# Kernel optimization log

Hardware: AMD Instinct MI355X
Metric: run time of the kernel (lower is better)

The kernel has to match this reference:

```python
import jax, jax.numpy as jnp
import numpy as np

M, K, N = 131072, 1024, 512


def setup_inputs() -> dict:
    key = jax.random.key(0)
    k1, k2, k3, k4, k5 = jax.random.split(key, 5)
    scale = 0.02
    return {
        "x": jax.random.normal(k1, (M, K), dtype=jnp.float32),
        "w0": jax.random.uniform(k2, (K,), dtype=jnp.float32, minval=0.9, maxval=1.1),
        "w1": jax.random.normal(k3, (K, N), dtype=jnp.float32) * scale,
        "w2": jax.random.normal(k4, (K, N), dtype=jnp.float32) * scale,
        "w3": jax.random.normal(k5, (N, K), dtype=jnp.float32) * scale,
    }


def reference(x, w0, w1, w2, w3):
    # RMSNorm (no eps, matching the kernel): l = rsqrt(mean(x^2))
    l = jax.lax.rsqrt(jnp.sum(x * x, axis=-1) / K)          # [M]
    x1 = x * l[:, None] * w0[None, :]                        # [M, K]
    x2 = x1 @ w1                                             # gate   [M, N]
    y2 = x1 @ w2                                             # up     [M, N]
    x3 = jax.nn.silu(x2) * y2                                # SiLU-gate [M, N]
    out = x3 @ w3                                            # down   [M, K] (skip_connection=False)
    return out
```

## Files before the change

kernel.cpp:

```cpp
#include <hip/hip_runtime.h>
#include <cstdint>

typedef __attribute__((ext_vector_type(4))) float f32x4;
typedef __attribute__((ext_vector_type(8))) short bf16x8;
typedef __attribute__((ext_vector_type(4))) short bf16x4;

#define DEV static __device__ __forceinline__

DEV unsigned short f2bf(float f) {
    union { float f; unsigned int u; } v; v.f = f;
    unsigned int u = v.u;
    return (unsigned short)((u + 0x7FFFu + ((u >> 16) & 1u)) >> 16);
}

DEV void async_cp16(const void* g, void* l) {
    __builtin_amdgcn_global_load_lds(
        (const __attribute__((address_space(1))) unsigned int*)g,
        (__attribute__((address_space(3))) unsigned int*)l,
        16, 0, 0);
}

DEV void stage_half(const unsigned short* __restrict__ g, long kofs,
                    unsigned short* l, int tid, int gpitch) {
#pragma unroll
    for (int i = 0; i < 2; ++i) {
        int c = i * 512 + tid;
        int row = c >> 3;
        int ss = (c & 7) ^ (row & 7);
        async_cp16(g + (long)row * gpitch + kofs + ss * 8,
                   l + (i * 512 + (tid & 448)) * 8);
    }
}

DEV bf16x8 ldsrd(const unsigned short* base, int r, int q) {
    return *(const bf16x8*)&base[r * 64 + ((q ^ (r & 7)) << 3)];
}

template <int NT>
DEV void gemm256(const unsigned short* __restrict__ gA,
                 const unsigned short* __restrict__ gB,
                 const int gpitch, unsigned short* lds,
                 f32x4 (&acc)[8][4], const int tid) {
    const int lane = tid & 63;
    const int wv = tid >> 6;
    const int wr = wv >> 2;
    const int wcq = wv & 3;
    const int lhi = lane >> 4, llo = lane & 15;
    const int hb = wcq >> 1;
    const int br0 = (wcq & 1) * 64;

#define MG(AF, BF, KQ, RI0, CJ0)                                              \
    _Pragma("unroll") for (int i = 0; i < 4; ++i)                             \
    _Pragma("unroll") for (int j = 0; j < 2; ++j)                             \
        acc[RI0 + i][CJ0 + j] = __builtin_amdgcn_mfma_f32_16x16x32_bf16(      \
            AF[KQ][i], BF[KQ][j], acc[RI0 + i][CJ0 + j], 0, 0, 0);

    stage_half(gA, 0, lds + 0 * 8192, tid, gpitch);
    stage_half(gA + (long)128 * gpitch, 0, lds + 1 * 8192, tid, gpitch);
    stage_half(gB, 0, lds + 32768 + 0 * 8192, tid, gpitch);
    stage_half(gB + (long)128 * gpitch, 0, lds + 32768 + 1 * 8192, tid, gpitch);
    if (NT > 1) {
        stage_half(gA, 64, lds + 2 * 8192, tid, gpitch);
        asm volatile("s_waitcnt vmcnt(2)" ::: "memory");
    } else {
        asm volatile("s_waitcnt vmcnt(0)" ::: "memory");
    }
    __builtin_amdgcn_s_barrier();
    __builtin_amdgcn_sched_barrier(0);

    bf16x8 af0[2][4], af1[2][4], bf0[2][2], bf1[2][2];

    {
        const unsigned short* lA = lds + wr * 8192;
        const unsigned short* lB = lds + 32768 + hb * 8192;
#pragma unroll
        for (int i = 0; i < 4; ++i) af0[0][i] = ldsrd(lA, i * 16 + llo, lhi);
#pragma unroll
        for (int j = 0; j < 2; ++j) bf0[0][j] = ldsrd(lB, br0 + j * 16 + llo, lhi);
    }

    for (int kt = 0; kt < NT; ++kt) {
        const int cur = kt & 1, nxt = cur ^ 1;
        const unsigned short* lA  = lds + (cur * 2 + wr) * 8192;
        const unsigned short* lB  = lds + 32768 + (cur * 2 + hb) * 8192;
        const unsigned short* lAn = lds + (nxt * 2 + wr) * 8192;
        const unsigned short* lBn = lds + 32768 + (nxt * 2 + hb) * 8192;
        const bool pf1 = (kt + 1 < NT);
        const bool pf2 = (kt + 2 < NT);
        const long k1 = (long)(kt + 1) * 64;
        const long k2 = (long)(kt + 2) * 64;

#pragma unroll
        for (int i = 0; i < 4; ++i) af0[1][i] = ldsrd(lA, i * 16 + llo, 4 + lhi);
#pragma unroll
        for (int j = 0; j < 2; ++j) bf0[1][j] = ldsrd(lB, br0 + j * 16 + llo, 4 + lhi);
#pragma unroll
        for (int kq = 0; kq < 2; ++kq)
#pragma unroll
            for (int j = 0; j < 2; ++j)
                bf1[kq][j] = ldsrd(lB, br0 + 32 + j * 16 + llo, kq * 4 + lhi);
        if (pf1) {
            stage_half(gA + (long)128 * gpitch, k1, lds + (nxt * 2 + 1) * 8192, tid, gpitch);
            stage_half(gB, k1, lds + 32768 + (nxt * 2 + 0) * 8192, tid, gpitch);
            stage_half(gB + (long)128 * gpitch, k1, lds + 32768 + (nxt * 2 + 1) * 8192, tid, gpitch);
        }
        __builtin_amdgcn_s_setprio(1);
        MG(af0, bf0, 0, 0, 0)
        MG(af0, bf0, 1, 0, 0)
        __builtin_amdgcn_s_setprio(0);

        __builtin_amdgcn_s_setprio(1);
        MG(af0, bf1, 0, 0, 2)
        MG(af0, bf1, 1, 0, 2)
        __builtin_amdgcn_s_setprio(0);

#pragma unroll
        for (int kq = 0; kq < 2; ++kq)
#pragma unroll
            for (int i = 0; i < 4; ++i)
                af1[kq][i] = ldsrd(lA, 64 + i * 16 + llo, kq * 4 + lhi);
        __builtin_amdgcn_s_setprio(1);
        MG(af1, bf0, 0, 4, 0)
        MG(af1, bf0, 1, 4, 0)
        __builtin_amdgcn_s_setprio(0);
        asm volatile("s_waitcnt vmcnt(0)" ::: "memory");
        __builtin_amdgcn_s_barrier();
        __builtin_amdgcn_sched_barrier(0);

        if (pf1) {
#pragma unroll
            for (int i = 0; i < 4; ++i) af0[0][i] = ldsrd(lAn, i * 16 + llo, lhi);
#pragma unroll
            for (int j = 0; j < 2; ++j) bf0[0][j] = ldsrd(lBn, br0 + j * 16 + llo, lhi);
        }
        if (pf2) stage_half(gA, k2, lds + (cur * 2 + 0) * 8192, tid, gpitch);
        __builtin_amdgcn_s_setprio(1);
        MG(af1, bf1, 0, 4, 2)
        MG(af1, bf1, 1, 4, 2)
        __builtin_amdgcn_s_setprio(0);
    }
#undef MG
}

__global__ void prep_w(const float* __restrict__ w0, const float* __restrict__ w1,
                       const float* __restrict__ w2, const float* __restrict__ w3,
                       unsigned short* __restrict__ w12t, unsigned short* __restrict__ w3t) {
    int t = blockIdx.x * 256 + threadIdx.x;
    if (t < 1048576) {
        int n = t >> 10, k = t & 1023;
        const float* src = (n & 1) ? w2 : w1;
        w12t[t] = f2bf(w0[k] * src[k * 512 + (n >> 1)]);
    } else {
        int idx = t - 1048576;
        int j = idx >> 9, n = idx & 511;
        w3t[idx] = f2bf(w3[n * 1024 + j]);
    }
}

__global__ __launch_bounds__(256)
void prep_x(const float* __restrict__ x, unsigned short* __restrict__ xb) {
    const int wv = threadIdx.x >> 6, lane = threadIdx.x & 63;
    const int stride = gridDim.x * 4;
    for (int row = blockIdx.x * 4 + wv; row < 131072; row += stride) {
        const float* xr = x + (long)row * 1024;
        f32x4 v[4];
        float s = 0.f;
#pragma unroll
        for (int c = 0; c < 4; ++c) {
            v[c] = *(const f32x4*)(xr + c * 256 + lane * 4);
            s += v[c].x * v[c].x + v[c].y * v[c].y + v[c].z * v[c].z + v[c].w * v[c].w;
        }
#pragma unroll
        for (int off = 32; off > 0; off >>= 1) s += __shfl_xor(s, off, 64);
        float l = rsqrtf(s * (1.0f / 1024.0f));
        unsigned short* xo = xb + (long)row * 1024;
#pragma unroll
        for (int c = 0; c < 4; ++c) {
            bf16x4 b;
            b.x = (short)f2bf(v[c].x * l);
            b.y = (short)f2bf(v[c].y * l);
            b.z = (short)f2bf(v[c].z * l);
            b.w = (short)f2bf(v[c].w * l);
            *(bf16x4*)(xo + c * 256 + lane * 4) = b;
        }
    }
}

__global__ __launch_bounds__(512, 2)
void gate_gemm(const unsigned short* __restrict__ xb,
               const unsigned short* __restrict__ w12t,
               unsigned short* __restrict__ x3) {
    __shared__ unsigned short lds[65536];
    const int tid = threadIdx.x;
    const int lane = tid & 63;
    const int wv = tid >> 6;
    const int wr = wv >> 2, wcq = wv & 3;
    const int lhi = lane >> 4, llo = lane & 15;

    int bid = blockIdx.x;
    int wgid = (bid & 7) * 256 + (bid >> 3);
    const int mt = wgid >> 2, nt = wgid & 3;

    f32x4 acc[8][4];
#pragma unroll
    for (int i = 0; i < 8; ++i)
#pragma unroll
        for (int j = 0; j < 4; ++j) acc[i][j] = (f32x4){0.f, 0.f, 0.f, 0.f};

    gemm256<16>(xb + (long)mt * 256 * 1024, w12t + (long)nt * 256 * 1024,
                1024, lds, acc, tid);

#pragma unroll
    for (int ri = 0; ri < 8; ++ri)
#pragma unroll
        for (int rr = 0; rr < 4; ++rr) {
            int R = wr * 128 + ri * 16 + lhi * 4 + rr;
#pragma unroll
            for (int cj = 0; cj < 4; ++cj) {
                float v = acc[ri][cj][rr];
                float p = __shfl_xor(v, 1, 64);
                float g = (lane & 1) ? p : v;
                float u = (lane & 1) ? v : p;
                float s = (g / (1.0f + __expf(-g))) * u;
                if (!(lane & 1))
                    lds[R * 136 + wcq * 32 + cj * 8 + (llo >> 1)] = f2bf(s);
            }
        }
    __syncthreads();
    unsigned short* xg = x3 + (long)(mt * 256) * 512 + nt * 128;
#pragma unroll
    for (int i = 0; i < 8; ++i) {
        int c = i * 512 + tid;
        int row = c >> 4, ch = c & 15;
        *(bf16x8*)(xg + (long)row * 512 + ch * 8) = *(const bf16x8*)&lds[row * 136 + ch * 8];
    }
}

__global__ __launch_bounds__(512, 2)
void down_gemm(const unsigned short* __restrict__ x3,
               const unsigned short* __restrict__ w3t,
               float* __restrict__ out) {
    __shared__ unsigned short lds[65536];
    const int tid = threadIdx.x;
    const int lane = tid & 63;
    const int wv = tid >> 6;
    const int wr = wv >> 2, wcq = wv & 3;
    const int lhi = lane >> 4, llo = lane & 15;

    int bid = blockIdx.x;
    int wgid = (bid & 7) * 256 + (bid >> 3);
    const int mt = wgid >> 2, nt = wgid & 3;

    f32x4 acc[8][4];
#pragma unroll
    for (int i = 0; i < 8; ++i)
#pragma unroll
        for (int j = 0; j < 4; ++j) acc[i][j] = (f32x4){0.f, 0.f, 0.f, 0.f};

    gemm256<8>(x3 + (long)mt * 256 * 512, w3t + (long)nt * 256 * 512,
               512, lds, acc, tid);

    float* op = out + (long)(mt * 256) * 1024 + nt * 256;
#pragma unroll
    for (int ri = 0; ri < 8; ++ri)
#pragma unroll
        for (int rr = 0; rr < 4; ++rr) {
            int R = wr * 128 + ri * 16 + lhi * 4 + rr;
#pragma unroll
            for (int cj = 0; cj < 4; ++cj)
                op[(long)R * 1024 + wcq * 64 + cj * 16 + llo] = acc[ri][cj][rr];
        }
}

extern "C" void kernel_launch(void* const* d_in, const int* in_sizes, int n_in,
                              void* d_out, int out_size, void* d_ws, size_t ws_size,
                              hipStream_t stream) {
    const float* x  = (const float*)d_in[0];
    const float* w0 = (const float*)d_in[1];
    const float* w1 = (const float*)d_in[2];
    const float* w2 = (const float*)d_in[3];
    const float* w3 = (const float*)d_in[4];
    float* out = (float*)d_out;

    unsigned short* w12t = (unsigned short*)d_ws;
    unsigned short* w3t  = w12t + 1024 * 1024;
    unsigned short* x3   = w3t + 1024 * 512;
    unsigned short* xb   = x3 + (size_t)131072 * 512;

    prep_w<<<dim3(6144), dim3(256), 0, stream>>>(w0, w1, w2, w3, w12t, w3t);
    prep_x<<<dim3(2048), dim3(256), 0, stream>>>(x, xb);
    gate_gemm<<<dim3(2048), dim3(512), 0, stream>>>(xb, w12t, x3);
    down_gemm<<<dim3(2048), dim3(512), 0, stream>>>(x3, w3t, out);
}
```

Measured before the change: 710.4 us.

## Restructure GEMM main loop into unrolled ping-pong schedule with barriered quadrant phases

Replaces the per-k-tile loop with a two-tile unrolled loop using fixed LDS buffer pointers. Each 64-wide k tile is split into four MFMA quadrant phases, each preceded by LDS fragment reads, one global-to-LDS staging call, a barrier and an lgkmcnt wait. The aim is to interleave global loads, LDS reads and MFMAs across waves in a fixed order, in the style of ping-pong scheduling. It adds many more barriers per tile, which can stall waves, and it assumes NT is even.

Measured after the change: 697.7 us. Within noise of the previous version (-1.8%).

```diff
diff --git a/kernel.cpp b/kernel.cpp
--- a/kernel.cpp
+++ b/kernel.cpp
@@ -49,97 +49,115 @@
     const int hb = wcq >> 1;
     const int br0 = (wcq & 1) * 64;
 
-#define MG(AF, BF, KQ, RI0, CJ0)                                              \
+    const unsigned short* lA0 = lds + (0 * 2 + wr) * 8192;
+    const unsigned short* lA1 = lds + (1 * 2 + wr) * 8192;
+    const unsigned short* lB0 = lds + 32768 + (0 * 2 + hb) * 8192;
+    const unsigned short* lB1 = lds + 32768 + (1 * 2 + hb) * 8192;
+
+#define MG(AF, BF, RI0, CJ0)                                                  \
+    _Pragma("unroll") for (int kq = 0; kq < 2; ++kq)                          \
     _Pragma("unroll") for (int i = 0; i < 4; ++i)                             \
     _Pragma("unroll") for (int j = 0; j < 2; ++j)                             \
         acc[RI0 + i][CJ0 + j] = __builtin_amdgcn_mfma_f32_16x16x32_bf16(      \
-            AF[KQ][i], BF[KQ][j], acc[RI0 + i][CJ0 + j], 0, 0, 0);
-
-    stage_half(gA, 0, lds + 0 * 8192, tid, gpitch);
-    stage_half(gA + (long)128 * gpitch, 0, lds + 1 * 8192, tid, gpitch);
-    stage_half(gB, 0, lds + 32768 + 0 * 8192, tid, gpitch);
-    stage_half(gB + (long)128 * gpitch, 0, lds + 32768 + 1 * 8192, tid, gpitch);
-    if (NT > 1) {
-        stage_half(gA, 64, lds + 2 * 8192, tid, gpitch);
-        asm volatile("s_waitcnt vmcnt(2)" ::: "memory");
-    } else {
-        asm volatile("s_waitcnt vmcnt(0)" ::: "memory");
-    }
-    __builtin_amdgcn_s_barrier();
-    __builtin_amdgcn_sched_barrier(0);
+            AF[kq][i], BF[kq][j], acc[RI0 + i][CJ0 + j], 0, 0, 0);
+
+#define RD_AF0(L) _Pragma("unroll") for (int kq = 0; kq < 2; ++kq)            \
+    _Pragma("unroll") for (int i = 0; i < 4; ++i)                             \
+        af0[kq][i] = ldsrd(L, i * 16 + llo, kq * 4 + lhi);
+#define RD_AF1(L) _Pragma("unroll") for (int kq = 0; kq < 2; ++kq)            \
+    _Pragma("unroll") for (int i = 0; i < 4; ++i)                             \
+        af1[kq][i] = ldsrd(L, 64 + i * 16 + llo, kq * 4 + lhi);
+#define RD_BF0(L) _Pragma("unroll") for (int kq = 0; kq < 2; ++kq)            \
+    _Pragma("unroll") for (int j = 0; j < 2; ++j)                             \
+        bf0[kq][j] = ldsrd(L, br0 + j * 16 + llo, kq * 4 + lhi);
+#define RD_BF1(L) _Pragma("unroll") for (int kq = 0; kq < 2; ++kq)            \
+    _Pragma("unroll") for (int j = 0; j < 2; ++j)                             \
+        bf1[kq][j] = ldsrd(L, br0 + 32 + j * 16 + llo, kq * 4 + lhi);
+
+#define SA0(BUF, K) stage_half(gA, K, lds + ((BUF) * 2 + 0) * 8192, tid, gpitch);
+#define SA1(BUF, K) stage_half(gA + (long)128 * gpitch, K, lds + ((BUF) * 2 + 1) * 8192, tid, gpitch);
+#define SB0(BUF, K) stage_half(gB, K, lds + 32768 + ((BUF) * 2 + 0) * 8192, tid, gpitch);
+#define SB1(BUF, K) stage_half(gB + (long)128 * gpitch, K, lds + 32768 + ((BUF) * 2 + 1) * 8192, tid, gpitch);
+
+#define BAR __builtin_amdgcn_s_barrier();
+#define SCB __builtin_amdgcn_sched_barrier(0);
+#define LGKM0 asm volatile("s_waitcnt lgkmcnt(0)");
+#define P1 __builtin_amdgcn_s_setprio(1);
+#define P0 __builtin_amdgcn_s_setprio(0);
+#define VM2 asm volatile("s_waitcnt vmcnt(2)" ::: "memory");
+#define VM0 asm volatile("s_waitcnt vmcnt(0)" ::: "memory");
+
+    SA0(0, 0) SA1(0, 0) SB0(0, 0) SB1(0, 0)
+    SA0(1, 64)
+    VM2
+    BAR
 
     bf16x8 af0[2][4], af1[2][4], bf0[2][2], bf1[2][2];
 
-    {
-        const unsigned short* lA = lds + wr * 8192;
-        const unsigned short* lB = lds + 32768 + hb * 8192;
-#pragma unroll
-        for (int i = 0; i < 4; ++i) af0[0][i] = ldsrd(lA, i * 16 + llo, lhi);
-#pragma unroll
-        for (int j = 0; j < 2; ++j) bf0[0][j] = ldsrd(lB, br0 + j * 16 + llo, lhi);
-    }
-
-    for (int kt = 0; kt < NT; ++kt) {
-        const int cur = kt & 1, nxt = cur ^ 1;
-        const unsigned short* lA  = lds + (cur * 2 + wr) * 8192;
-        const unsigned short* lB  = lds + 32768 + (cur * 2 + hb) * 8192;
-        const unsigned short* lAn = lds + (nxt * 2 + wr) * 8192;
-        const unsigned short* lBn = lds + 32768 + (nxt * 2 + hb) * 8192;
-        const bool pf1 = (kt + 1 < NT);
-        const bool pf2 = (kt + 2 < NT);
-        const long k1 = (long)(kt + 1) * 64;
-        const long k2 = (long)(kt + 2) * 64;
-
-#pragma unroll
-        for (int i = 0; i < 4; ++i) af0[1][i] = ldsrd(lA, i * 16 + llo, 4 + lhi);
-#pragma unroll
-        for (int j = 0; j < 2; ++j) bf0[1][j] = ldsrd(lB, br0 + j * 16 + llo, 4 + lhi);
-#pragma unroll
-        for (int kq = 0; kq < 2; ++kq)
-#pragma unroll
-            for (int j = 0; j < 2; ++j)
-                bf1[kq][j] = ldsrd(lB, br0 + 32 + j * 16 + llo, kq * 4 + lhi);
-        if (pf1) {
-            stage_half(gA + (long)128 * gpitch, k1, lds + (nxt * 2 + 1) * 8192, tid, gpitch);
-            stage_half(gB, k1, lds + 32768 + (nxt * 2 + 0) * 8192, tid, gpitch);
-            stage_half(gB + (long)128 * gpitch, k1, lds + 32768 + (nxt * 2 + 1) * 8192, tid, gpitch);
-        }
-        __builtin_amdgcn_s_setprio(1);
-        MG(af0, bf0, 0, 0, 0)
-        MG(af0, bf0, 1, 0, 0)
-        __builtin_amdgcn_s_setprio(0);
-
-        __builtin_amdgcn_s_setprio(1);
-        MG(af0, bf1, 0, 0, 2)
-        MG(af0, bf1, 1, 0, 2)
-        __builtin_amdgcn_s_setprio(0);
-
-#pragma unroll
-        for (int kq = 0; kq < 2; ++kq)
-#pragma unroll
-            for (int i = 0; i < 4; ++i)
-                af1[kq][i] = ldsrd(lA, 64 + i * 16 + llo, kq * 4 + lhi);
-        __builtin_amdgcn_s_setprio(1);
-        MG(af1, bf0, 0, 4, 0)
-        MG(af1, bf0, 1, 4, 0)
-        __builtin_amdgcn_s_setprio(0);
-        asm volatile("s_waitcnt vmcnt(0)" ::: "memory");
-        __builtin_amdgcn_s_barrier();
-        __builtin_amdgcn_sched_barrier(0);
-
-        if (pf1) {
-#pragma unroll
-            for (int i = 0; i < 4; ++i) af0[0][i] = ldsrd(lAn, i * 16 + llo, lhi);
-#pragma unroll
-            for (int j = 0; j < 2; ++j) bf0[0][j] = ldsrd(lBn, br0 + j * 16 + llo, lhi);
-        }
-        if (pf2) stage_half(gA, k2, lds + (cur * 2 + 0) * 8192, tid, gpitch);
-        __builtin_amdgcn_s_setprio(1);
-        MG(af1, bf1, 0, 4, 2)
-        MG(af1, bf1, 1, 4, 2)
-        __builtin_amdgcn_s_setprio(0);
+    for (int it = 0; it < NT / 2; ++it) {
+        const long kO  = (long)(2 * it + 1) * 64;
+        const long kE2 = (long)(2 * it + 2) * 64;
+        const long kO2 = (long)(2 * it + 3) * 64;
+        const bool pf = (it + 1 < NT / 2);
+
+        RD_AF0(lA0) RD_BF0(lB0)
+        SA1(1, kO)
+        BAR LGKM0 SCB
+        P1 MG(af0, bf0, 0, 0) P0
+        BAR
+        RD_BF1(lB0)
+        SB0(1, kO)
+        BAR LGKM0 SCB
+        P1 MG(af0, bf1, 0, 2) P0
+        BAR
+        RD_AF1(lA0)
+        SB1(1, kO)
+        BAR LGKM0 SCB
+        P1 MG(af1, bf0, 4, 0) P0
+        BAR
+        if (pf) { SA0(0, kE2) }
+        BAR
+        P1 MG(af1, bf1, 4, 2) P0
+        if (pf) { VM2 } else { VM0 }
+        BAR SCB
+
+        RD_AF0(lA1) RD_BF0(lB1)
+        if (pf) { SA1(0, kE2) }
+        BAR LGKM0 SCB
+        P1 MG(af0, bf0, 0, 0) P0
+        BAR
+        RD_BF1(lB1)
+        if (pf) { SB0(0, kE2) }
+        BAR LGKM0 SCB
+        P1 MG(af0, bf1, 0, 2) P0
+        BAR
+        RD_AF1(lA1)
+        if (pf) { SB1(0, kE2) }
+        BAR LGKM0 SCB
+        P1 MG(af1, bf0, 4, 0) P0
+        BAR
+        if (pf) { SA0(1, kO2) }
+        BAR
+        P1 MG(af1, bf1, 4, 2) P0
+        if (pf) { VM2 }
+        BAR SCB
     }
 #undef MG
+#undef RD_AF0
+#undef RD_AF1
+#undef RD_BF0
+#undef RD_BF1
+#undef SA0
+#undef SA1
+#undef SB0
+#undef SB1
+#undef BAR
+#undef SCB
+#undef LGKM0
+#undef P1
+#undef P0
+#undef VM2
+#undef VM0
 }
 
 __global__ void prep_w(const float* __restrict__ w0, const float* __restrict__ w1,
```
